# Kernel optimization log

Measured on AMD Instinct MI355X. Metric: run time of the kernel, lower is better.

The kernel has to match this reference:

```python
import jax, jax.numpy as jnp
import numpy as np

LN_EPS = 1e-5

def setup_inputs() -> dict:
    key = jax.random.key(0)
    B, S, D = 4, 2048, 1024
    ks = jax.random.split(key, 8)
    sc = 1.0 / np.sqrt(D)
    inp = {
        'x': jax.random.normal(ks[0], (B, S, D), jnp.float32),
        'Wq': jax.random.normal(ks[1], (D, D), jnp.float32) * sc,
        'bq': jnp.zeros((D,), jnp.float32),
        'Wk': jax.random.normal(ks[2], (D, D), jnp.float32) * sc,
        'bk': jnp.zeros((D,), jnp.float32),
        'Wv': jax.random.normal(ks[3], (D, D), jnp.float32) * sc,
        'bv': jnp.zeros((D,), jnp.float32),
        'Wo': jax.random.normal(ks[4], (D, D), jnp.float32) * sc,
        'bo': jnp.zeros((D,), jnp.float32),
        'Wg_val': jax.random.normal(ks[5], (D, D), jnp.float32) * sc,
        'bg_val': jnp.zeros((D,), jnp.float32),
        'Wg_gate': jax.random.normal(ks[6], (D, D), jnp.float32) * sc,
        'bg_gate': jnp.zeros((D,), jnp.float32),
        'gamma': jnp.ones((D,), jnp.float32),
        'beta': jnp.zeros((D,), jnp.float32),
    }
    return inp


def reference(x, Wq, bq, Wk, bk, Wv, bv, Wo, bo, Wg_val, bg_val, Wg_gate, bg_gate, gamma, beta):
    # x: [B,S,D]
    q = jnp.einsum('bsd,de->bse', x, Wq) + bq
    k = jnp.einsum('bsd,de->bse', x, Wk) + bk
    v = jnp.einsum('bsd,de->bse', x, Wv) + bv
    scale = 1.0 / jnp.sqrt(jnp.asarray(q.shape[-1], q.dtype))
    qk = jnp.einsum('bqe,bke->bqk', q, k) * scale  # [B,S,S]
    a = jax.nn.softmax(qk, axis=-1)
    out = jnp.einsum('bqk,bke->bqe', a, v)
    out = jnp.einsum('bse,ed->bsd', out, Wo) + bo
    # GLU residual on q, then LayerNorm
    glu = (jnp.einsum('bse,ed->bsd', q, Wg_val) + bg_val) * jax.nn.sigmoid(jnp.einsum('bse,ed->bsd', q, Wg_gate) + bg_gate)
    out = out + glu
    mu = jnp.mean(out, axis=-1, keepdims=True)
    var = jnp.var(out, axis=-1, keepdims=True)
    out = (out - mu) * jax.lax.rsqrt(var + LN_EPS) * gamma + beta
    return out
```

## Files before the change

kernel.cpp:

```cpp
#include <hip/hip_runtime.h>
#include <hip/hip_bf16.h>
#include <cstdint>


typedef __bf16 bf16x8 __attribute__((ext_vector_type(8)));
typedef __bf16 bf16x4 __attribute__((ext_vector_type(4)));
typedef float f32x4 __attribute__((ext_vector_type(4)));

#define SYNC() do { asm volatile("" ::: "memory"); __builtin_amdgcn_s_barrier(); asm volatile("" ::: "memory"); } while (0)
#define WAITV(n) asm volatile("s_waitcnt vmcnt(" #n ")" ::: "memory")

__device__ __forceinline__ void gload_lds16(const void* g, void* l) {
    __builtin_amdgcn_global_load_lds(
        (__attribute__((address_space(1))) void*)(uintptr_t)g,
        (__attribute__((address_space(3))) void*)(uintptr_t)l,
        16, 0, 0);
}

#define STAGE(buf, isB, half, kt)                                                        \
    do {                                                                                 \
        const __hip_bfloat16* g_ = (isB) ? gB : gA;                                      \
        const int ld_ = (isB) ? ldb : lda;                                               \
        char* l_ = smem + (buf) * 65536 + (isB) * 32768 + (half) * 16384;                \
        gload_lds16(g_ + (long)((half) * 128 + r0) * ld_ + (kt) * 64 + s0 * 8, l_ + tid * 16);        \
        gload_lds16(g_ + (long)((half) * 128 + r1) * ld_ + (kt) * 64 + s1 * 8, l_ + 8192 + tid * 16); \
    } while (0)
#define LDA_(dst, buf, mh, mi, kk)                                                       \
    do {                                                                                 \
        const int lr_ = wm * 64 + (mi) * 16 + fr;                                        \
        const int sl_ = ((kk) * 4 + kg) ^ (lr_ & 7);                                     \
        dst = *(const bf16x8*)(smem + (buf) * 65536 + (mh) * 16384 + lr_ * 128 + sl_ * 16); \
    } while (0)
#define LDB_(dst, buf, nh, ni, kk)                                                       \
    do {                                                                                 \
        const int lr_ = wn * 32 + (ni) * 16 + fr;                                        \
        const int sl_ = ((kk) * 4 + kg) ^ (lr_ & 7);                                     \
        dst = *(const bf16x8*)(smem + (buf) * 65536 + 32768 + (nh) * 16384 + lr_ * 128 + sl_ * 16); \
    } while (0)
#define MFMA_QUAD(mh, nh)                                                                \
    do {                                                                                 \
        __builtin_amdgcn_s_setprio(1);                                                   \
        _Pragma("unroll")                                                                \
        for (int mi = 0; mi < 4; ++mi)                                                   \
            _Pragma("unroll")                                                            \
            for (int ni = 0; ni < 2; ++ni)                                               \
                _Pragma("unroll")                                                        \
                for (int kk = 0; kk < 2; ++kk)                                           \
                    acc[mh][nh][mi][ni] = __builtin_amdgcn_mfma_f32_16x16x32_bf16(       \
                        av[mi][kk], bv[ni][kk], acc[mh][nh][mi][ni], 0, 0, 0);           \
        __builtin_amdgcn_s_setprio(0);                                                   \
    } while (0)

#define GEMM256_BODY(NT)                                                                 \
    STAGE(0, 0, 0, 0);                                                                   \
    STAGE(0, 1, 0, 0);                                                                   \
    STAGE(0, 1, 1, 0);                                                                   \
    STAGE(0, 0, 1, 0);                                                                   \
    WAITV(4);                                                                            \
    SYNC();                                                                              \
    for (int t = 0; t < (NT) - 1; ++t) {                                                 \
        const int c = t & 1;                                                             \
        _Pragma("unroll")                                                                \
        for (int mi = 0; mi < 4; ++mi) { LDA_(av[mi][0], c, 0, mi, 0); LDA_(av[mi][1], c, 0, mi, 1); } \
        _Pragma("unroll")                                                                \
        for (int ni = 0; ni < 2; ++ni) { LDB_(bv[ni][0], c, 0, ni, 0); LDB_(bv[ni][1], c, 0, ni, 1); } \
        STAGE(c ^ 1, 0, 0, t + 1);                                                       \
        MFMA_QUAD(0, 0);                                                                 \
        WAITV(4);                                                                        \
        SYNC();                                                                          \
        _Pragma("unroll")                                                                \
        for (int ni = 0; ni < 2; ++ni) { LDB_(bv[ni][0], c, 1, ni, 0); LDB_(bv[ni][1], c, 1, ni, 1); } \
        STAGE(c ^ 1, 1, 0, t + 1);                                                       \
        MFMA_QUAD(0, 1);                                                                 \
        WAITV(4);                                                                        \
        SYNC();                                                                          \
        _Pragma("unroll")                                                                \
        for (int mi = 0; mi < 4; ++mi) { LDA_(av[mi][0], c, 1, mi, 0); LDA_(av[mi][1], c, 1, mi, 1); } \
        STAGE(c ^ 1, 1, 1, t + 1);                                                       \
        MFMA_QUAD(1, 1);                                                                 \
        SYNC();                                                                          \
        _Pragma("unroll")                                                                \
        for (int ni = 0; ni < 2; ++ni) { LDB_(bv[ni][0], c, 0, ni, 0); LDB_(bv[ni][1], c, 0, ni, 1); } \
        STAGE(c ^ 1, 0, 1, t + 1);                                                       \
        MFMA_QUAD(1, 0);                                                                 \
        WAITV(4);                                                                        \
        SYNC();                                                                          \
    }                                                                                    \
    {                                                                                    \
        const int c = ((NT) - 1) & 1;                                                    \
        _Pragma("unroll")                                                                \
        for (int mi = 0; mi < 4; ++mi) { LDA_(av[mi][0], c, 0, mi, 0); LDA_(av[mi][1], c, 0, mi, 1); } \
        _Pragma("unroll")                                                                \
        for (int ni = 0; ni < 2; ++ni) { LDB_(bv[ni][0], c, 0, ni, 0); LDB_(bv[ni][1], c, 0, ni, 1); } \
        MFMA_QUAD(0, 0);                                                                 \
        WAITV(2);                                                                        \
        SYNC();                                                                          \
        _Pragma("unroll")                                                                \
        for (int ni = 0; ni < 2; ++ni) { LDB_(bv[ni][0], c, 1, ni, 0); LDB_(bv[ni][1], c, 1, ni, 1); } \
        MFMA_QUAD(0, 1);                                                                 \
        WAITV(0);                                                                        \
        SYNC();                                                                          \
        _Pragma("unroll")                                                                \
        for (int mi = 0; mi < 4; ++mi) { LDA_(av[mi][0], c, 1, mi, 0); LDA_(av[mi][1], c, 1, mi, 1); } \
        MFMA_QUAD(1, 1);                                                                 \
        _Pragma("unroll")                                                                \
        for (int ni = 0; ni < 2; ++ni) { LDB_(bv[ni][0], c, 0, ni, 0); LDB_(bv[ni][1], c, 0, ni, 1); } \
        MFMA_QUAD(1, 0);                                                                 \
    }

template <int EPI>
__global__ __launch_bounds__(512, 1) void gemm256(
    const __hip_bfloat16* __restrict__ A1, int lda1,
    const __hip_bfloat16* __restrict__ A2, int lda2, int nsplit,
    const __hip_bfloat16* __restrict__ Bt,
    __hip_bfloat16* __restrict__ Cout, const float* __restrict__ bias, float scale,
    int K, int ldb, int ldc,
    long strideA, long strideB, long strideC)
{
    __shared__ __align__(16) char smem[131072];

    const int b = blockIdx.z;
    const int tid = threadIdx.x;
    const int lane = tid & 63;
    const int wm = (tid >> 6) & 1;
    const int wn = (tid >> 6) >> 1;

    const bool sel2 = ((int)blockIdx.y * 256) >= nsplit;
    const __hip_bfloat16* A = sel2 ? A2 : A1;
    const int lda = sel2 ? lda2 : lda1;

    const __hip_bfloat16* gA = A + (long)b * strideA + (long)blockIdx.x * 256 * lda;
    const __hip_bfloat16* gB = Bt + (long)b * strideB + (long)blockIdx.y * 256 * ldb;

    const int r0 = tid >> 3;
    const int s0 = (tid & 7) ^ (r0 & 7);
    const int r1 = r0 + 64;
    const int s1 = (tid & 7) ^ (r1 & 7);
    const int fr = lane & 15;
    const int kg = lane >> 4;

    f32x4 acc[2][2][4][2];
#pragma unroll
    for (int mh = 0; mh < 2; ++mh)
#pragma unroll
        for (int nh = 0; nh < 2; ++nh)
#pragma unroll
            for (int mi = 0; mi < 4; ++mi)
#pragma unroll
                for (int ni = 0; ni < 2; ++ni) acc[mh][nh][mi][ni] = {0.f, 0.f, 0.f, 0.f};
    bf16x8 av[4][2], bv[2][2];

    const int NT = K >> 6;
    GEMM256_BODY(NT)

    const long row0 = (long)blockIdx.x * 256 + wm * 64 + (lane >> 4) * 4;
    const long col0 = (long)blockIdx.y * 256 + wn * 32 + (lane & 15);
#pragma unroll
    for (int mh = 0; mh < 2; ++mh) {
#pragma unroll
        for (int nh = 0; nh < 2; ++nh) {
#pragma unroll
            for (int ni = 0; ni < 2; ++ni) {
                const long col = col0 + nh * 128 + ni * 16;
                const float bval = (EPI == 0 && bias != nullptr) ? bias[col] : 0.f;
#pragma unroll
                for (int mi = 0; mi < 4; ++mi) {
                    const long row = row0 + mh * 128 + mi * 16;
#pragma unroll
                    for (int i = 0; i < 4; ++i) {
                        const float v = (EPI == 1) ? acc[mh][nh][mi][ni][i] * scale
                                                   : acc[mh][nh][mi][ni][i] + bval;
                        Cout[(long)b * strideC + (row + i) * (long)ldc + col] = __float2bfloat16(v);
                    }
                }
            }
        }
    }
}

__global__ __launch_bounds__(512, 1) void gemm256_dual(
    const __hip_bfloat16* __restrict__ wvT,
    const __hip_bfloat16* __restrict__ xb,
    const __hip_bfloat16* __restrict__ Qp,
    const __hip_bfloat16* __restrict__ wggT,
    __hip_bfloat16* __restrict__ vt,
    __hip_bfloat16* __restrict__ T1G,
    const float* __restrict__ bv,
    const float* __restrict__ bgg)
{
    __shared__ __align__(16) char smem[131072];

    const int bid = blockIdx.x;
    const bool isVt = bid < 128;
    const int tid = threadIdx.x;
    const int lane = tid & 63;
    const int wm = (tid >> 6) & 1;
    const int wn = (tid >> 6) >> 1;

    int mx, my, lda, ldb;
    const __hip_bfloat16 *Aop, *Bop;
    if (isVt) { mx = bid >> 5; my = bid & 31; Aop = wvT; lda = 1024; Bop = xb;   ldb = 1024; }
    else { const int t2 = bid - 128; mx = t2 >> 2; my = t2 & 3; Aop = Qp; lda = 2048; Bop = wggT; ldb = 1024; }

    const __hip_bfloat16* gA = Aop + (long)mx * 256 * lda;
    const __hip_bfloat16* gB = Bop + (long)my * 256 * ldb;

    const int r0 = tid >> 3;
    const int s0 = (tid & 7) ^ (r0 & 7);
    const int r1 = r0 + 64;
    const int s1 = (tid & 7) ^ (r1 & 7);
    const int fr = lane & 15;
    const int kg = lane >> 4;

    f32x4 acc[2][2][4][2];
#pragma unroll
    for (int mh = 0; mh < 2; ++mh)
#pragma unroll
        for (int nh = 0; nh < 2; ++nh)
#pragma unroll
            for (int mi = 0; mi < 4; ++mi)
#pragma unroll
                for (int ni = 0; ni < 2; ++ni) acc[mh][nh][mi][ni] = {0.f, 0.f, 0.f, 0.f};
    bf16x8 av[4][2], bv2[2][2];
    #define bv bv2
    GEMM256_BODY(16)
    #undef bv

    const long row0 = (long)mx * 256 + wm * 64 + (lane >> 4) * 4;
    const long col0 = (long)my * 256 + wn * 32 + (lane & 15);
    if (isVt) {
#pragma unroll
        for (int mh = 0; mh < 2; ++mh)
#pragma unroll
            for (int nh = 0; nh < 2; ++nh)
#pragma unroll
                for (int ni = 0; ni < 2; ++ni) {
                    const long col = col0 + nh * 128 + ni * 16;
                    const long vb = col >> 11, vs = col & 2047;
#pragma unroll
                    for (int mi = 0; mi < 4; ++mi) {
#pragma unroll
                        for (int i = 0; i < 4; ++i) {
                            const long row = row0 + mh * 128 + mi * 16 + i;
                            vt[(vb << 21) + row * 2048 + vs] =
                                __float2bfloat16(acc[mh][nh][mi][ni][i] + bv[row]);
                        }
                    }
                }
    } else {
#pragma unroll
        for (int mh = 0; mh < 2; ++mh)
#pragma unroll
            for (int nh = 0; nh < 2; ++nh)
#pragma unroll
                for (int ni = 0; ni < 2; ++ni) {
                    const long col = col0 + nh * 128 + ni * 16;
                    const float bval = bgg[col];
#pragma unroll
                    for (int mi = 0; mi < 4; ++mi) {
                        const long row = row0 + mh * 128 + mi * 16;
#pragma unroll
                        for (int i = 0; i < 4; ++i)
                            T1G[(row + i) * 3072 + 2048 + col] =
                                __float2bfloat16(acc[mh][nh][mi][ni][i] + bval);
                    }
                }
    }
}

__global__ __launch_bounds__(512, 1) void gemm_tn128(
    const __hip_bfloat16* __restrict__ A, int lda,
    const __hip_bfloat16* __restrict__ Bt,
    __hip_bfloat16* __restrict__ Cout, const float* __restrict__ bias,
    int K, int ldb, int ldc,
    long strideA, long strideB, long strideC)
{
    __shared__ __align__(16) char smem[147456];

    const int b = blockIdx.z;
    const int tid = threadIdx.x;
    const int lane = tid & 63;
    const int wid = tid >> 6;
    const int wm = wid & 3;
    const int wn = wid >> 2;

    const __hip_bfloat16* gA = A + (long)b * strideA + (long)blockIdx.x * 256 * lda;
    const __hip_bfloat16* gB = Bt + (long)b * strideB + (long)blockIdx.y * 128 * ldb;

    const int r0 = tid >> 3, r1 = r0 + 64;
    const int s0 = (tid & 7) ^ (r0 & 7);
    const int s1 = (tid & 7) ^ (r1 & 7);

#define STG_A(base_, h_, kt_)                                                                              \
    do {                                                                                                   \
        gload_lds16(gA + (long)((h_) * 128 + r0) * lda + (kt_) * 64 + s0 * 8, (base_) + (h_) * 16384 + tid * 16);        \
        gload_lds16(gA + (long)((h_) * 128 + r1) * lda + (kt_) * 64 + s1 * 8, (base_) + (h_) * 16384 + 8192 + tid * 16); \
    } while (0)
#define STG_B(base_, kt_)                                                                                  \
    do {                                                                                                   \
        gload_lds16(gB + (long)r0 * ldb + (kt_) * 64 + s0 * 8, (base_) + 32768 + tid * 16);                \
        gload_lds16(gB + (long)r1 * ldb + (kt_) * 64 + s1 * 8, (base_) + 32768 + 8192 + tid * 16);         \
    } while (0)

    const int fr = lane & 15;
    const int kg = lane >> 4;

#define LD_A(dst, base_, mi_, kk_)                                                        \
    do {                                                                                  \
        const int row_ = wm * 64 + (mi_) * 16 + fr;                                       \
        const int sl_ = ((kk_) * 4 + kg) ^ (row_ & 7);                                    \
        dst = *(const bf16x8*)((base_) + row_ * 128 + sl_ * 16);                          \
    } while (0)
#define LD_B(dst, base_, ni_, kk_)                                                        \
    do {                                                                                  \
        const int row_ = wn * 64 + (ni_) * 16 + fr;                                       \
        const int sl_ = ((kk_) * 4 + kg) ^ (row_ & 7);                                    \
        dst = *(const bf16x8*)((base_) + 32768 + row_ * 128 + sl_ * 16);                  \
    } while (0)

    f32x4 acc[4][4];
#pragma unroll
    for (int mi = 0; mi < 4; ++mi)
#pragma unroll
        for (int ni = 0; ni < 4; ++ni) acc[mi][ni] = {0.f, 0.f, 0.f, 0.f};

    const int NT = K >> 6;

    STG_A(smem, 0, 0); STG_A(smem, 1, 0); STG_B(smem, 0);
    STG_A(smem + 49152, 0, 1); STG_A(smem + 49152, 1, 1); STG_B(smem + 49152, 1);
    WAITV(6);
    SYNC();

    int bi = 0;
    for (int t = 0; t < NT; ++t) {
        char* base = smem + bi * 49152;
        if (t + 2 < NT) {
            int bs = bi + 2; if (bs >= 3) bs -= 3;
            char* sb = smem + bs * 49152;
            STG_A(sb, 0, t + 2); STG_A(sb, 1, t + 2); STG_B(sb, t + 2);
        }
        bf16x8 av[4], bvv[4];
#pragma unroll
        for (int kk = 0; kk < 2; ++kk) {
#pragma unroll
            for (int mi = 0; mi < 4; ++mi) LD_A(av[mi], base, mi, kk);
#pragma unroll
            for (int ni = 0; ni < 4; ++ni) LD_B(bvv[ni], base, ni, kk);
            __builtin_amdgcn_s_setprio(1);
#pragma unroll
            for (int mi = 0; mi < 4; ++mi)
#pragma unroll
                for (int ni = 0; ni < 4; ++ni)
                    acc[mi][ni] = __builtin_amdgcn_mfma_f32_16x16x32_bf16(av[mi], bvv[ni], acc[mi][ni], 0, 0, 0);
            __builtin_amdgcn_s_setprio(0);
        }
        if (t + 2 < NT) { WAITV(6); SYNC(); }
        else if (t + 1 < NT) { WAITV(0); SYNC(); }
        bi = (bi + 1 == 3) ? 0 : bi + 1;
    }

    const long row0 = (long)blockIdx.x * 256 + wm * 64 + (lane >> 4) * 4;
    const long col0 = (long)blockIdx.y * 128 + wn * 64 + (lane & 15);
#pragma unroll
    for (int ni = 0; ni < 4; ++ni) {
        const long col = col0 + ni * 16;
        const float bval = (bias != nullptr) ? bias[col] : 0.f;
#pragma unroll
        for (int mi = 0; mi < 4; ++mi) {
            const long row = row0 + mi * 16;
#pragma unroll
            for (int i = 0; i < 4; ++i)
                Cout[(long)b * strideC + (row + i) * (long)ldc + col] = __float2bfloat16(acc[mi][ni][i] + bval);
        }
    }
#undef STG_A
#undef STG_B
#undef LD_A
#undef LD_B
}

__global__ __launch_bounds__(256) void transpose6(
    const float* __restrict__ W0, const float* __restrict__ W1, const float* __restrict__ W2,
    const float* __restrict__ W3, const float* __restrict__ W4, const float* __restrict__ W5,
    __hip_bfloat16* __restrict__ dst)
{
    __shared__ float tile[32][33];
    const int z = blockIdx.z;
    const float* pin = (z == 0) ? W0 : (z == 1) ? W1 : (z == 2) ? W2 : (z == 3) ? W3 : (z == 4) ? W4 : W5;
    __hip_bfloat16* pout = dst + (long)z * 1024 * 1024;
    const int tx = threadIdx.x, ty = threadIdx.y;
    const int c0 = blockIdx.x * 32, r0 = blockIdx.y * 32;
#pragma unroll
    for (int j = 0; j < 4; ++j)
        tile[ty + j * 8][tx] = pin[(long)(r0 + ty + j * 8) * 1024 + c0 + tx];
    __syncthreads();
#pragma unroll
    for (int j = 0; j < 4; ++j)
        pout[(long)(c0 + ty + j * 8) * 1024 + r0 + tx] = __float2bfloat16(tile[tx][ty + j * 8]);
}

__global__ __launch_bounds__(256) void f32_to_bf16_vec(
    const float* __restrict__ in, __hip_bfloat16* __restrict__ out, long n4)
{
    const long i = (long)blockIdx.x * 256 + threadIdx.x;
    if (i >= n4) return;
    const float4 v = ((const float4*)in)[i];
    union { __hip_bfloat16 h[4]; ushort4 u; } cv;
    cv.h[0] = __float2bfloat16(v.x);
    cv.h[1] = __float2bfloat16(v.y);
    cv.h[2] = __float2bfloat16(v.z);
    cv.h[3] = __float2bfloat16(v.w);
    ((ushort4*)out)[i] = cv.u;
}

__global__ __launch_bounds__(256) void concat_bias(
    const float* __restrict__ bq, const float* __restrict__ bk, const float* __restrict__ bv,
    const float* __restrict__ bo, const float* __restrict__ bgv, const float* __restrict__ bgg,
    float* __restrict__ out)
{
    const int i = blockIdx.x * 256 + threadIdx.x;
    float v;
    if (i < 1024) v = bq[i];
    else if (i < 2048) v = bk[i - 1024];
    else if (i < 3072) v = bv[i - 2048];
    else if (i < 4096) v = bo[i - 3072];
    else if (i < 5120) v = bgv[i - 4096];
    else v = bgg[i - 5120];
    out[i] = v;
}

__global__ __launch_bounds__(256) void softmax_kernel(
    const __hip_bfloat16* __restrict__ S, __hip_bfloat16* __restrict__ P)
{
    const long row = blockIdx.x;
    const __hip_bfloat16* s = S + row * 2048;
    __hip_bfloat16* p = P + row * 2048;
    const int t = threadIdx.x;
    const bf16x8 v8 = *(const bf16x8*)(s + t * 8);
    float v[8];
    float mx = -1e30f;
#pragma unroll
    for (int j = 0; j < 8; ++j) { v[j] = (float)v8[j]; mx = fmaxf(mx, v[j]); }
#pragma unroll
    for (int off = 32; off; off >>= 1) mx = fmaxf(mx, __shfl_xor(mx, off));
    __shared__ float wred[4];
    __shared__ float wsum[4];
    const int w = t >> 6;
    if ((t & 63) == 0) wred[w] = mx;
    __syncthreads();
    mx = fmaxf(fmaxf(wred[0], wred[1]), fmaxf(wred[2], wred[3]));
    float sum = 0.f;
#pragma unroll
    for (int j = 0; j < 8; ++j) { v[j] = __expf(v[j] - mx); sum += v[j]; }
#pragma unroll
    for (int off = 32; off; off >>= 1) sum += __shfl_xor(sum, off);
    if ((t & 63) == 0) wsum[w] = sum;
    __syncthreads();
    sum = wsum[0] + wsum[1] + wsum[2] + wsum[3];
    const float inv = 1.0f / sum;
    bf16x8 o8;
#pragma unroll
    for (int j = 0; j < 8; ++j) o8[j] = (__bf16)(v[j] * inv);
    *(bf16x8*)(p + t * 8) = o8;
}

__global__ __launch_bounds__(256) void glu_ln_kernel(
    const __hip_bfloat16* __restrict__ T1G,
    const float* __restrict__ gamma, const float* __restrict__ beta, float* __restrict__ out)
{
    const long row = blockIdx.x;
    const __hip_bfloat16* pr = T1G + row * 3072;
    const int t = threadIdx.x;
    const int c0 = t * 4;
    const bf16x4 t1 = *(const bf16x4*)(pr + c0);
    const bf16x4 gv = *(const bf16x4*)(pr + 1024 + c0);
    const bf16x4 gg = *(const bf16x4*)(pr + 2048 + c0);
    float y[4];
    float s = 0.f, ss = 0.f;
#pragma unroll
    for (int j = 0; j < 4; ++j) {
        const float g = (float)gv[j] * (1.0f / (1.0f + __expf(-(float)gg[j])));
        const float val = (float)t1[j] + g;
        y[j] = val; s += val; ss += val * val;
    }
#pragma unroll
    for (int off = 32; off; off >>= 1) { s += __shfl_xor(s, off); ss += __shfl_xor(ss, off); }
    __shared__ float rs[4], rss[4];
    const int w = t >> 6;
    if ((t & 63) == 0) { rs[w] = s; rss[w] = ss; }
    __syncthreads();
    s = rs[0] + rs[1] + rs[2] + rs[3];
    ss = rss[0] + rss[1] + rss[2] + rss[3];
    const float mu = s * (1.0f / 1024.0f);
    const float var = ss * (1.0f / 1024.0f) - mu * mu;
    const float r = rsqrtf(var + 1e-5f);
    const float4 gm = *(const float4*)(gamma + c0);
    const float4 bt = *(const float4*)(beta + c0);
    float4 o;
    o.x = (y[0] - mu) * r * gm.x + bt.x;
    o.y = (y[1] - mu) * r * gm.y + bt.y;
    o.z = (y[2] - mu) * r * gm.z + bt.z;
    o.w = (y[3] - mu) * r * gm.w + bt.w;
    *(float4*)(out + row * 1024 + c0) = o;
}

extern "C" void kernel_launch(void* const* d_in, const int* in_sizes, int n_in,
                              void* d_out, int out_size, void* d_ws, size_t ws_size,
                              hipStream_t stream)
{
    const int B = 4, S = 2048, D = 1024;
    const float* x    = (const float*)d_in[0];
    const float* Wq   = (const float*)d_in[1];
    const float* bq   = (const float*)d_in[2];
    const float* Wk   = (const float*)d_in[3];
    const float* bk   = (const float*)d_in[4];
    const float* Wv   = (const float*)d_in[5];
    const float* bv   = (const float*)d_in[6];
    const float* Wo   = (const float*)d_in[7];
    const float* bo   = (const float*)d_in[8];
    const float* Wgv  = (const float*)d_in[9];
    const float* bgv  = (const float*)d_in[10];
    const float* Wgg  = (const float*)d_in[11];
    const float* bgg  = (const float*)d_in[12];
    const float* gamma = (const float*)d_in[13];
    const float* beta  = (const float*)d_in[14];
    float* out = (float*)d_out;

    char* ws = (char*)d_ws;
    size_t off = 0;
    auto take = [&](size_t bytes) { char* p = ws + off; off += (bytes + 255) & ~(size_t)255; return p; };

    __hip_bfloat16* wcat   = (__hip_bfloat16*)take((size_t)6 * D * D * 2);
    float*          bcat   = (float*)take((size_t)6 * D * 4);
    __hip_bfloat16* xb     = (__hip_bfloat16*)take((size_t)B * S * D * 2);
    __hip_bfloat16* QKb    = (__hip_bfloat16*)take((size_t)B * S * 2 * D * 2);
    __hip_bfloat16* Vtb    = (__hip_bfloat16*)take((size_t)B * S * D * 2);
    __hip_bfloat16* scoresb = (__hip_bfloat16*)take((size_t)B * S * S * 2);
    __hip_bfloat16* Pb     = (__hip_bfloat16*)take((size_t)B * S * S * 2);
    __hip_bfloat16* Oatt   = (__hip_bfloat16*)take((size_t)B * S * D * 2);
    __hip_bfloat16* T1G    = (__hip_bfloat16*)take((size_t)B * S * 3 * D * 2);

    const long SD = (long)S * D, SS = (long)S * S, S2D = (long)S * 2 * D;
    const float att_scale = 0.03125f;
    const __hip_bfloat16* Qb = QKb;
    const __hip_bfloat16* Kb = QKb + D;

    f32_to_bf16_vec<<<dim3((unsigned)((long)B * S * D / 4 / 256)), dim3(256), 0, stream>>>(x, xb, (long)B * S * D / 4);
    transpose6<<<dim3(D / 32, D / 32, 6), dim3(32, 8), 0, stream>>>(Wq, Wk, Wv, Wo, Wgv, Wgg, wcat);
    concat_bias<<<dim3(24), dim3(256), 0, stream>>>(bq, bk, bv, bo, bgv, bgg, bcat);

    gemm256<0><<<dim3(B * S / 256, 2 * D / 256, 1), dim3(512), 0, stream>>>(
        xb, D, xb, D, 1 << 30, wcat, QKb, bcat, 1.f,
        D, D, 2 * D, 0, 0, 0);

    gemm256_dual<<<dim3(256), dim3(512), 0, stream>>>(
        wcat + (size_t)2 * D * D, xb, QKb, wcat + (size_t)5 * D * D,
        Vtb, T1G, bcat + 2 * D, bcat + 5 * D);

    gemm256<1><<<dim3(S / 256, S / 256, B), dim3(512), 0, stream>>>(
        Qb, 2 * D, Qb, 2 * D, 1 << 30, Kb, scoresb, nullptr, att_scale,
        D, 2 * D, S, S2D, S2D, SS);

    softmax_kernel<<<dim3(B * S), dim3(256), 0, stream>>>(scoresb, Pb);

    gemm_tn128<<<dim3(S / 256, D / 128, B), dim3(512), 0, stream>>>(
        Pb, S, Vtb, Oatt, nullptr, S, S, D, SS, SD, SD);

    gemm256<0><<<dim3(B * S / 256, 2 * D / 256, 1), dim3(512), 0, stream>>>(
        Oatt, D, QKb, 2 * D, D, wcat + (size_t)3 * D * D, T1G, bcat + 3 * D, 1.f,
        D, D, 3 * D, 0, 0, 0);

    glu_ln_kernel<<<dim3(B * S), dim3(256), 0, stream>>>(T1G, gamma, beta, out);
}
```

Baseline: 226.0 us.

## Switch GEMM pipelines to 32-wide K tiles with 4-stage LDS ring buffer

```diff
diff --git a/kernel.cpp b/kernel.cpp
--- a/kernel.cpp
+++ b/kernel.cpp
@@ -10,102 +10,79 @@
 #define SYNC() do { asm volatile("" ::: "memory"); __builtin_amdgcn_s_barrier(); asm volatile("" ::: "memory"); } while (0)
 #define WAITV(n) asm volatile("s_waitcnt vmcnt(" #n ")" ::: "memory")
 
-__device__ __forceinline__ void gload_lds16(const void* g, void* l) {
+__device__ __forceinline__ void gload16(const void* g, void* l) {
     __builtin_amdgcn_global_load_lds(
         (__attribute__((address_space(1))) void*)(uintptr_t)g,
         (__attribute__((address_space(3))) void*)(uintptr_t)l,
         16, 0, 0);
 }
 
-#define STAGE(buf, isB, half, kt)                                                        \
+#define G256_STAGE(buf, isB, half, kt)                                                   \
     do {                                                                                 \
         const __hip_bfloat16* g_ = (isB) ? gB : gA;                                      \
         const int ld_ = (isB) ? ldb : lda;                                               \
-        char* l_ = smem + (buf) * 65536 + (isB) * 32768 + (half) * 16384;                \
-        gload_lds16(g_ + (long)((half) * 128 + r0) * ld_ + (kt) * 64 + s0 * 8, l_ + tid * 16);        \
-        gload_lds16(g_ + (long)((half) * 128 + r1) * ld_ + (kt) * 64 + s1 * 8, l_ + 8192 + tid * 16); \
+        gload16(g_ + (long)((half) * 128 + r0) * ld_ + (kt) * 32 + s0 * 8,               \
+                smem + (buf) * 32768 + (isB) * 16384 + (half) * 8192 + tid * 16);        \
     } while (0)
-#define LDA_(dst, buf, mh, mi, kk)                                                       \
+#define G256_LDA(dst, buf, mh, mi)                                                       \
     do {                                                                                 \
-        const int lr_ = wm * 64 + (mi) * 16 + fr;                                        \
-        const int sl_ = ((kk) * 4 + kg) ^ (lr_ & 7);                                     \
-        dst = *(const bf16x8*)(smem + (buf) * 65536 + (mh) * 16384 + lr_ * 128 + sl_ * 16); \
+        const int row_ = wm * 64 + (mi) * 16 + fr;                                       \
+        const int sl_ = kg ^ ((row_ >> 1) & 3);                                          \
+        dst = *(const bf16x8*)(smem + (buf) * 32768 + (mh) * 8192 + row_ * 64 + sl_ * 16); \
     } while (0)
-#define LDB_(dst, buf, nh, ni, kk)                                                       \
+#define G256_LDB(dst, buf, nh, ni)                                                       \
     do {                                                                                 \
-        const int lr_ = wn * 32 + (ni) * 16 + fr;                                        \
-        const int sl_ = ((kk) * 4 + kg) ^ (lr_ & 7);                                     \
-        dst = *(const bf16x8*)(smem + (buf) * 65536 + 32768 + (nh) * 16384 + lr_ * 128 + sl_ * 16); \
+        const int row_ = wn * 32 + (ni) * 16 + fr;                                       \
+        const int sl_ = kg ^ ((row_ >> 1) & 3);                                          \
+        dst = *(const bf16x8*)(smem + (buf) * 32768 + 16384 + (nh) * 8192 + row_ * 64 + sl_ * 16); \
     } while (0)
-#define MFMA_QUAD(mh, nh)                                                                \
-    do {                                                                                 \
+
+#define GEMM256_BODY(NT)                                                                 \
+    for (int tt = 0; tt < 3; ++tt) {                                                     \
+        G256_STAGE(tt, 0, 0, tt); G256_STAGE(tt, 1, 0, tt);                              \
+        G256_STAGE(tt, 1, 1, tt); G256_STAGE(tt, 0, 1, tt);                              \
+    }                                                                                    \
+    WAITV(8);                                                                            \
+    SYNC();                                                                              \
+    for (int t = 0; t < (NT); ++t) {                                                     \
+        const int c = t & 3;                                                             \
+        const bool st = (t + 3 < (NT));                                                  \
+        const int sb = (t + 3) & 3;                                                      \
+        bf16x8 av[4], bv[2][2];                                                          \
+        _Pragma("unroll")                                                                \
+        for (int nh = 0; nh < 2; ++nh)                                                   \
+            _Pragma("unroll")                                                            \
+            for (int ni = 0; ni < 2; ++ni) G256_LDB(bv[nh][ni], c, nh, ni);              \
+        if (st) { G256_STAGE(sb, 0, 0, t + 3); G256_STAGE(sb, 1, 0, t + 3); }            \
+        _Pragma("unroll")                                                                \
+        for (int mi = 0; mi < 4; ++mi) G256_LDA(av[mi], c, 0, mi);                       \
         __builtin_amdgcn_s_setprio(1);                                                   \
         _Pragma("unroll")                                                                \
         for (int mi = 0; mi < 4; ++mi)                                                   \
             _Pragma("unroll")                                                            \
-            for (int ni = 0; ni < 2; ++ni)                                               \
+            for (int nh = 0; nh < 2; ++nh)                                               \
                 _Pragma("unroll")                                                        \
-                for (int kk = 0; kk < 2; ++kk)                                           \
-                    acc[mh][nh][mi][ni] = __builtin_amdgcn_mfma_f32_16x16x32_bf16(       \
-                        av[mi][kk], bv[ni][kk], acc[mh][nh][mi][ni], 0, 0, 0);           \
+                for (int ni = 0; ni < 2; ++ni)                                           \
+                    acc[0][nh][mi][ni] = __builtin_amdgcn_mfma_f32_16x16x32_bf16(        \
+                        av[mi], bv[nh][ni], acc[0][nh][mi][ni], 0, 0, 0);                \
         __builtin_amdgcn_s_setprio(0);                                                   \
-    } while (0)
-
-#define GEMM256_BODY(NT)                                                                 \
-    STAGE(0, 0, 0, 0);                                                                   \
-    STAGE(0, 1, 0, 0);                                                                   \
-    STAGE(0, 1, 1, 0);                                                                   \
-    STAGE(0, 0, 1, 0);                                                                   \
-    WAITV(4);                                                                            \
-    SYNC();                                                                              \
-    for (int t = 0; t < (NT) - 1; ++t) {                                                 \
-        const int c = t & 1;                                                             \
+        if (st) { G256_STAGE(sb, 1, 1, t + 3); G256_STAGE(sb, 0, 1, t + 3); }            \
         _Pragma("unroll")                                                                \
-        for (int mi = 0; mi < 4; ++mi) { LDA_(av[mi][0], c, 0, mi, 0); LDA_(av[mi][1], c, 0, mi, 1); } \
+        for (int mi = 0; mi < 4; ++mi) G256_LDA(av[mi], c, 1, mi);                       \
+        __builtin_amdgcn_s_setprio(1);                                                   \
         _Pragma("unroll")                                                                \
-        for (int ni = 0; ni < 2; ++ni) { LDB_(bv[ni][0], c, 0, ni, 0); LDB_(bv[ni][1], c, 0, ni, 1); } \
-        STAGE(c ^ 1, 0, 0, t + 1);                                                       \
-        MFMA_QUAD(0, 0);                                                                 \
-        WAITV(4);                                                                        \
-        SYNC();                                                                          \
-        _Pragma("unroll")                                                                \
-        for (int ni = 0; ni < 2; ++ni) { LDB_(bv[ni][0], c, 1, ni, 0); LDB_(bv[ni][1], c, 1, ni, 1); } \
-        STAGE(c ^ 1, 1, 0, t + 1);                                                       \
-        MFMA_QUAD(0, 1);                                                                 \
-        WAITV(4);                                                                        \
-        SYNC();                                                                          \
-        _Pragma("unroll")                                                                \
-        for (int mi = 0; mi < 4; ++mi) { LDA_(av[mi][0], c, 1, mi, 0); LDA_(av[mi][1], c, 1, mi, 1); } \
-        STAGE(c ^ 1, 1, 1, t + 1);                                                       \
-        MFMA_QUAD(1, 1);                                                                 \
-        SYNC();                                                                          \
-        _Pragma("unroll")                                                                \
-        for (int ni = 0; ni < 2; ++ni) { LDB_(bv[ni][0], c, 0, ni, 0); LDB_(bv[ni][1], c, 0, ni, 1); } \
-        STAGE(c ^ 1, 0, 1, t + 1);                                                       \
-        MFMA_QUAD(1, 0);                                                                 \
-        WAITV(4);                                                                        \
-        SYNC();                                                                          \
-    }                                                                                    \
-    {                                                                                    \
-        const int c = ((NT) - 1) & 1;                                                    \
-        _Pragma("unroll")                                                                \
-        for (int mi = 0; mi < 4; ++mi) { LDA_(av[mi][0], c, 0, mi, 0); LDA_(av[mi][1], c, 0, mi, 1); } \
-        _Pragma("unroll")                                                                \
-        for (int ni = 0; ni < 2; ++ni) { LDB_(bv[ni][0], c, 0, ni, 0); LDB_(bv[ni][1], c, 0, ni, 1); } \
-        MFMA_QUAD(0, 0);                                                                 \
-        WAITV(2);                                                                        \
-        SYNC();                                                                          \
-        _Pragma("unroll")                                                                \
-        for (int ni = 0; ni < 2; ++ni) { LDB_(bv[ni][0], c, 1, ni, 0); LDB_(bv[ni][1], c, 1, ni, 1); } \
-        MFMA_QUAD(0, 1);                                                                 \
-        WAITV(0);                                                                        \
-        SYNC();                                                                          \
-        _Pragma("unroll")                                                                \
-        for (int mi = 0; mi < 4; ++mi) { LDA_(av[mi][0], c, 1, mi, 0); LDA_(av[mi][1], c, 1, mi, 1); } \
-        MFMA_QUAD(1, 1);                                                                 \
-        _Pragma("unroll")                                                                \
-        for (int ni = 0; ni < 2; ++ni) { LDB_(bv[ni][0], c, 0, ni, 0); LDB_(bv[ni][1], c, 0, ni, 1); } \
-        MFMA_QUAD(1, 0);                                                                 \
+        for (int mi = 0; mi < 4; ++mi)                                                   \
+            _Pragma("unroll")                                                            \
+            for (int nh = 0; nh < 2; ++nh)                                               \
+                _Pragma("unroll")                                                        \
+                for (int ni = 0; ni < 2; ++ni)                                           \
+                    acc[1][nh][mi][ni] = __builtin_amdgcn_mfma_f32_16x16x32_bf16(        \
+                        av[mi], bv[nh][ni], acc[1][nh][mi][ni], 0, 0, 0);                \
+        __builtin_amdgcn_s_setprio(0);                                                   \
+        const int rem = (NT) - 1 - t;                                                    \
+        if (rem >= 3) { WAITV(8); SYNC(); }                                              \
+        else if (rem == 2) { WAITV(4); SYNC(); }                                         \
+        else if (rem == 1) { WAITV(0); SYNC(); }                                         \
     }
 
 template <int EPI>
@@ -132,10 +109,8 @@
     const __hip_bfloat16* gA = A + (long)b * strideA + (long)blockIdx.x * 256 * lda;
     const __hip_bfloat16* gB = Bt + (long)b * strideB + (long)blockIdx.y * 256 * ldb;
 
-    const int r0 = tid >> 3;
-    const int s0 = (tid & 7) ^ (r0 & 7);
-    const int r1 = r0 + 64;
-    const int s1 = (tid & 7) ^ (r1 & 7);
+    const int r0 = tid >> 2;
+    const int s0 = (tid & 3) ^ ((r0 >> 1) & 3);
     const int fr = lane & 15;
     const int kg = lane >> 4;
 
@@ -148,9 +123,8 @@
             for (int mi = 0; mi < 4; ++mi)
 #pragma unroll
                 for (int ni = 0; ni < 2; ++ni) acc[mh][nh][mi][ni] = {0.f, 0.f, 0.f, 0.f};
-    bf16x8 av[4][2], bv[2][2];
-
-    const int NT = K >> 6;
+
+    const int NT = K >> 5;
     GEMM256_BODY(NT)
 
     const long row0 = (long)blockIdx.x * 256 + wm * 64 + (lane >> 4) * 4;
@@ -179,14 +153,10 @@
 }
 
 __global__ __launch_bounds__(512, 1) void gemm256_dual(
-    const __hip_bfloat16* __restrict__ wvT,
-    const __hip_bfloat16* __restrict__ xb,
-    const __hip_bfloat16* __restrict__ Qp,
-    const __hip_bfloat16* __restrict__ wggT,
-    __hip_bfloat16* __restrict__ vt,
-    __hip_bfloat16* __restrict__ T1G,
-    const float* __restrict__ bv,
-    const float* __restrict__ bgg)
+    const __hip_bfloat16* __restrict__ wvT, const __hip_bfloat16* __restrict__ xb,
+    const __hip_bfloat16* __restrict__ Qp, const __hip_bfloat16* __restrict__ wggT,
+    __hip_bfloat16* __restrict__ vt, __hip_bfloat16* __restrict__ T1G,
+    const float* __restrict__ bvp, const float* __restrict__ bgg)
 {
     __shared__ __align__(16) char smem[131072];
 
@@ -205,10 +175,8 @@
     const __hip_bfloat16* gA = Aop + (long)mx * 256 * lda;
     const __hip_bfloat16* gB = Bop + (long)my * 256 * ldb;
 
-    const int r0 = tid >> 3;
-    const int s0 = (tid & 7) ^ (r0 & 7);
-    const int r1 = r0 + 64;
-    const int s1 = (tid & 7) ^ (r1 & 7);
+    const int r0 = tid >> 2;
+    const int s0 = (tid & 3) ^ ((r0 >> 1) & 3);
     const int fr = lane & 15;
     const int kg = lane >> 4;
 
@@ -221,10 +189,8 @@
             for (int mi = 0; mi < 4; ++mi)
 #pragma unroll
                 for (int ni = 0; ni < 2; ++ni) acc[mh][nh][mi][ni] = {0.f, 0.f, 0.f, 0.f};
-    bf16x8 av[4][2], bv2[2][2];
-    #define bv bv2
-    GEMM256_BODY(16)
-    #undef bv
+
+    GEMM256_BODY(32)
 
     const long row0 = (long)mx * 256 + wm * 64 + (lane >> 4) * 4;
     const long col0 = (long)my * 256 + wn * 32 + (lane & 15);
@@ -243,7 +209,7 @@
                         for (int i = 0; i < 4; ++i) {
                             const long row = row0 + mh * 128 + mi * 16 + i;
                             vt[(vb << 21) + row * 2048 + vs] =
-                                __float2bfloat16(acc[mh][nh][mi][ni][i] + bv[row]);
+                                __float2bfloat16(acc[mh][nh][mi][ni][i] + bvp[row]);
                         }
                     }
                 }
@@ -275,7 +241,7 @@
     int K, int ldb, int ldc,
     long strideA, long strideB, long strideC)
 {
-    __shared__ __align__(16) char smem[147456];
+    __shared__ __align__(16) char smem[98304];
 
     const int b = blockIdx.z;
     const int tid = threadIdx.x;
@@ -287,35 +253,29 @@
     const __hip_bfloat16* gA = A + (long)b * strideA + (long)blockIdx.x * 256 * lda;
     const __hip_bfloat16* gB = Bt + (long)b * strideB + (long)blockIdx.y * 128 * ldb;
 
-    const int r0 = tid >> 3, r1 = r0 + 64;
-    const int s0 = (tid & 7) ^ (r0 & 7);
-    const int s1 = (tid & 7) ^ (r1 & 7);
-
-#define STG_A(base_, h_, kt_)                                                                              \
-    do {                                                                                                   \
-        gload_lds16(gA + (long)((h_) * 128 + r0) * lda + (kt_) * 64 + s0 * 8, (base_) + (h_) * 16384 + tid * 16);        \
-        gload_lds16(gA + (long)((h_) * 128 + r1) * lda + (kt_) * 64 + s1 * 8, (base_) + (h_) * 16384 + 8192 + tid * 16); \
-    } while (0)
-#define STG_B(base_, kt_)                                                                                  \
-    do {                                                                                                   \
-        gload_lds16(gB + (long)r0 * ldb + (kt_) * 64 + s0 * 8, (base_) + 32768 + tid * 16);                \
-        gload_lds16(gB + (long)r1 * ldb + (kt_) * 64 + s1 * 8, (base_) + 32768 + 8192 + tid * 16);         \
-    } while (0)
-
+    const int r0 = tid >> 2;
+    const int s0 = (tid & 3) ^ ((r0 >> 1) & 3);
     const int fr = lane & 15;
     const int kg = lane >> 4;
 
-#define LD_A(dst, base_, mi_, kk_)                                                        \
+#define T128_STG(buf, kt)                                                                          \
+    do {                                                                                           \
+        char* base_ = smem + (buf) * 24576;                                                        \
+        gload16(gA + (long)r0 * lda + (kt) * 32 + s0 * 8, base_ + tid * 16);                       \
+        gload16(gA + (long)(128 + r0) * lda + (kt) * 32 + s0 * 8, base_ + 8192 + tid * 16);        \
+        gload16(gB + (long)r0 * ldb + (kt) * 32 + s0 * 8, base_ + 16384 + tid * 16);               \
+    } while (0)
+#define T128_LDA(dst, buf, mi_)                                                           \
     do {                                                                                  \
         const int row_ = wm * 64 + (mi_) * 16 + fr;                                       \
-        const int sl_ = ((kk_) * 4 + kg) ^ (row_ & 7);                                    \
-        dst = *(const bf16x8*)((base_) + row_ * 128 + sl_ * 16);                          \
+        const int sl_ = kg ^ ((row_ >> 1) & 3);                                           \
+        dst = *(const bf16x8*)(smem + (buf) * 24576 + row_ * 64 + sl_ * 16);              \
     } while (0)
-#define LD_B(dst, base_, ni_, kk_)                                                        \
+#define T128_LDB(dst, buf, ni_)                                                           \
     do {                                                                                  \
         const int row_ = wn * 64 + (ni_) * 16 + fr;                                       \
-        const int sl_ = ((kk_) * 4 + kg) ^ (row_ & 7);                                    \
-        dst = *(const bf16x8*)((base_) + 32768 + row_ * 128 + sl_ * 16);                  \
+        const int sl_ = kg ^ ((row_ >> 1) & 3);                                           \
+        dst = *(const bf16x8*)(smem + (buf) * 24576 + 16384 + row_ * 64 + sl_ * 16);      \
     } while (0)
 
     f32x4 acc[4][4];
@@ -324,39 +284,32 @@
 #pragma unroll
         for (int ni = 0; ni < 4; ++ni) acc[mi][ni] = {0.f, 0.f, 0.f, 0.f};
 
-    const int NT = K >> 6;
-
-    STG_A(smem, 0, 0); STG_A(smem, 1, 0); STG_B(smem, 0);
-    STG_A(smem + 49152, 0, 1); STG_A(smem + 49152, 1, 1); STG_B(smem + 49152, 1);
+    const int NT = K >> 5;
+
+    T128_STG(0, 0); T128_STG(1, 1); T128_STG(2, 2);
     WAITV(6);
     SYNC();
 
-    int bi = 0;
     for (int t = 0; t < NT; ++t) {
-        char* base = smem + bi * 49152;
-        if (t + 2 < NT) {
-            int bs = bi + 2; if (bs >= 3) bs -= 3;
-            char* sb = smem + bs * 49152;
-            STG_A(sb, 0, t + 2); STG_A(sb, 1, t + 2); STG_B(sb, t + 2);
-        }
-        bf16x8 av[4], bvv[4];
-#pragma unroll
-        for (int kk = 0; kk < 2; ++kk) {
-#pragma unroll
-            for (int mi = 0; mi < 4; ++mi) LD_A(av[mi], base, mi, kk);
-#pragma unroll
-            for (int ni = 0; ni < 4; ++ni) LD_B(bvv[ni], base, ni, kk);
-            __builtin_amdgcn_s_setprio(1);
-#pragma unroll
-            for (int mi = 0; mi < 4; ++mi)
-#pragma unroll
-                for (int ni = 0; ni < 4; ++ni)
-                    acc[mi][ni] = __builtin_amdgcn_mfma_f32_16x16x32_bf16(av[mi], bvv[ni], acc[mi][ni], 0, 0, 0);
-            __builtin_amdgcn_s_setprio(0);
-        }
-        if (t + 2 < NT) { WAITV(6); SYNC(); }
-        else if (t + 1 < NT) { WAITV(0); SYNC(); }
-        bi = (bi + 1 == 3) ? 0 : bi + 1;
+        const int c = t & 3;
+        const bool st = (t + 3 < NT);
+        bf16x8 av[4], bv[4];
+#pragma unroll
+        for (int ni = 0; ni < 4; ++ni) T128_LDB(bv[ni], c, ni);
+        if (st) T128_STG((t + 3) & 3, t + 3);
+#pragma unroll
+        for (int mi = 0; mi < 4; ++mi) T128_LDA(av[mi], c, mi);
+        __builtin_amdgcn_s_setprio(1);
+#pragma unroll
+        for (int mi = 0; mi < 4; ++mi)
+#pragma unroll
+            for (int ni = 0; ni < 4; ++ni)
+                acc[mi][ni] = __builtin_amdgcn_mfma_f32_16x16x32_bf16(av[mi], bv[ni], acc[mi][ni], 0, 0, 0);
+        __builtin_amdgcn_s_setprio(0);
+        const int rem = NT - 1 - t;
+        if (rem >= 3) { WAITV(6); SYNC(); }
+        else if (rem == 2) { WAITV(3); SYNC(); }
+        else if (rem == 1) { WAITV(0); SYNC(); }
     }
 
     const long row0 = (long)blockIdx.x * 256 + wm * 64 + (lane >> 4) * 4;
@@ -373,10 +326,9 @@
                 Cout[(long)b * strideC + (row + i) * (long)ldc + col] = __float2bfloat16(acc[mi][ni][i] + bval);
         }
     }
-#undef STG_A
-#undef STG_B
-#undef LD_A
-#undef LD_B
+#undef T128_STG
+#undef T128_LDA
+#undef T128_LDB
 }
 
 __global__ __launch_bounds__(256) void transpose6(
```

Measured after the change: 239.6 us. 1.06x slower.
